# Optimization experiments

Measured on AMD Instinct MI355X. Metric: run time of the kernel, lower is better.

The kernel has to match this reference:

```python
import jax, jax.numpy as jnp
import numpy as np
import math

BS, T, C, H, W = 2, 3, 128, 48, 48
NH, NL, NPT, KS = 8, 3, 4, 3
DH = C // NH
LQ = T * H * W


def conv2d(x, w, b):
    y = jax.lax.conv_general_dilated(x, w, (1, 1), 'SAME', dimension_numbers=('NCHW', 'OIHW', 'NCHW'))
    return y + b[None, :, None, None]


def bilinear_sample(img, x, y, zeros_pad):
    # img: (B, C, H, W); x, y: (B, Q) pixel coords. zeros_pad -> grid_sample padding_mode='zeros', else 'border'.
    B, Cc, Hh, Ww = img.shape
    x0 = jnp.floor(x); y0 = jnp.floor(y)
    wx = x - x0; wy = y - y0
    flat = img.reshape(B, Cc, Hh * Ww)
    def corner(xi, yi, wgt):
        if zeros_pad:
            wgt = wgt * ((xi >= 0) & (xi <= Ww - 1) & (yi >= 0) & (yi <= Hh - 1)).astype(img.dtype)
        xc = jnp.clip(xi, 0, Ww - 1).astype(jnp.int32)
        yc = jnp.clip(yi, 0, Hh - 1).astype(jnp.int32)
        g = jnp.take_along_axis(flat, (yc * Ww + xc)[:, None, :], axis=2)  # (B, C, Q)
        return g * wgt[:, None, :]
    return (corner(x0, y0, (1 - wx) * (1 - wy)) + corner(x0 + 1, y0, wx * (1 - wy))
            + corner(x0, y0 + 1, (1 - wx) * wy) + corner(x0 + 1, y0 + 1, wx * wy))


def warp_w_mask(x, flo):
    # grid_sample(border, align_corners=True): normalized coords round-trip to raw pixel coords grid+flow
    B, Cc, Hh, Ww = x.shape
    vx = (jnp.arange(Ww, dtype=x.dtype)[None, None, :] + flo[:, 0]).reshape(B, -1)
    vy = (jnp.arange(Hh, dtype=x.dtype)[None, :, None] + flo[:, 1]).reshape(B, -1)
    out = bilinear_sample(x, vx, vy, False).reshape(B, Cc, Hh, Ww)
    m = bilinear_sample(jnp.ones((B, 1, Hh, Ww), x.dtype), vx, vy, True).reshape(B, 1, Hh, Ww)
    m = jnp.where(m < 0.999, 0.0, 1.0).astype(x.dtype)
    return out * m


def flow_guid_offset(ff, fb, off):
    N = off.shape[0]
    off = off.reshape(N, NL, H * W, NH, NL, NPT, 2)
    ff01, ff12 = ff[:, 0], ff[:, 1]
    ff02 = ff01 + warp_w_mask(ff12, ff01)
    fb10, fb21 = fb[:, 0], fb[:, 1]
    fb20 = fb21 + warp_w_mask(fb10, fb21)
    seq = lambda f: f.transpose(0, 2, 3, 1).reshape(N, H * W, 2)
    z = jnp.zeros((N, H * W, 2), off.dtype)
    adds = jnp.stack([
        jnp.stack([z, seq(ff01), seq(ff02)], axis=2),
        jnp.stack([seq(fb10), z, seq(ff12)], axis=2),
        jnp.stack([seq(fb20), seq(fb21), z], axis=2)], axis=1)  # (N, 3, HW, 3, 2)
    off = off + adds[:, :, :, None, :, None, :]
    return off.reshape(N, LQ, NH, NL, NPT, 2)


def reference(query, input_flatten, reference_points, flow_forward, flow_backward,
              w_off, b_off, w_attn, b_attn, w_val, b_val, w_out, b_out,
              input_spatial_shapes, input_level_start_index, input_padding_mask):
    bs, t, c, h, w = query.shape
    N = bs
    value = conv2d(input_flatten.reshape(bs * t, c, h, w), w_val, b_val)
    off = conv2d(query.reshape(bs * t, c, h, w), w_off, b_off)
    attn = conv2d(query.reshape(bs * t, c, h, w), w_attn, b_attn)
    tohw = lambda x: x.reshape(bs, t, -1, h * w).transpose(0, 1, 3, 2).reshape(bs, t * h * w, -1)
    value, off, attn = tohw(value), tohw(off), tohw(attn)
    value = jnp.where(input_padding_mask[..., None], 0.0, value)
    value = value.reshape(N, t * h * w, NH, DH)
    off = off.reshape(N, LQ, NH, NL, NPT, 2)
    off = flow_guid_offset(flow_forward, flow_backward, off)
    attn = jax.nn.softmax(attn.reshape(N, LQ, NH, NL * NPT), axis=-1).reshape(N, LQ, NH, NL, NPT)
    normalizer = jnp.stack([input_spatial_shapes[:, 1], input_spatial_shapes[:, 0]], -1).astype(query.dtype)
    loc = reference_points[:, :, None, :, None, :] + off / normalizer[None, None, None, :, None, :]
    # multi-level deformable sampling: grid_sample(bilinear, zeros padding, align_corners=False)
    vb = value.reshape(N, NL, h * w, NH, DH).transpose(0, 1, 3, 4, 2).reshape(N * NL * NH, DH, h, w)
    px = (loc[..., 0] * w - 0.5).transpose(0, 3, 2, 1, 4).reshape(N * NL * NH, LQ * NPT)
    py = (loc[..., 1] * h - 0.5).transpose(0, 3, 2, 1, 4).reshape(N * NL * NH, LQ * NPT)
    samp = bilinear_sample(vb, px, py, True).reshape(N, NL, NH, DH, LQ, NPT)
    out = jnp.einsum('nlhdqp,nqhlp->nqhd', samp, attn).reshape(N, LQ, c)
    out = out.reshape(bs, t, h, w, c).transpose(0, 1, 4, 2, 3).reshape(bs * t, c, h, w)
    out = conv2d(out, w_out, b_out).reshape(bs, t, c, h, w)
    return out


def setup_inputs():
    key = jax.random.key(0)
    ks = jax.random.split(key, 9)
    query = jax.random.normal(ks[0], (BS, T, C, H, W), jnp.float32)
    input_flatten = jax.random.normal(ks[1], (BS, T, C, H, W), jnp.float32)
    reference_points = jax.random.uniform(ks[2], (BS, LQ, NL, 2), jnp.float32)
    flow_forward = jax.random.normal(ks[3], (BS, 2, 2, H, W), jnp.float32) * 2.0
    flow_backward = jax.random.normal(ks[4], (BS, 2, 2, H, W), jnp.float32) * 2.0
    co = NH * NL * NPT * 2
    w_off = jax.random.normal(ks[5], (co, C, KS, KS), jnp.float32) * 0.01
    thetas = np.arange(NH, dtype=np.float32) * (2.0 * math.pi / NH)
    g = np.stack([np.cos(thetas), np.sin(thetas)], -1)
    g = g / np.abs(g).max(-1, keepdims=True)
    g = np.tile(g.reshape(NH, 1, 1, 2), (1, NL, NPT, 1)) * (np.arange(NPT, dtype=np.float32) + 1.0).reshape(1, 1, NPT, 1)
    b_off = jnp.asarray(g.reshape(-1))
    ca = NH * NL * NPT
    w_attn = jax.random.normal(ks[6], (ca, C, KS, KS), jnp.float32) * 0.01
    b_attn = jnp.zeros((ca,), jnp.float32)
    s = 1.0 / np.sqrt(C * KS * KS)
    w_val = jax.random.normal(ks[7], (C, C, KS, KS), jnp.float32) * s
    b_val = jnp.zeros((C,), jnp.float32)
    w_out = jax.random.normal(ks[8], (C, C, KS, KS), jnp.float32) * s
    b_out = jnp.zeros((C,), jnp.float32)
    input_spatial_shapes = jnp.array([[H, W]] * NL, jnp.int32)
    input_level_start_index = jnp.array([0, H * W, 2 * H * W], jnp.int32)
    input_padding_mask = jnp.zeros((BS, LQ), bool)
    return {'query': query, 'input_flatten': input_flatten, 'reference_points': reference_points,
            'flow_forward': flow_forward, 'flow_backward': flow_backward,
            'w_off': w_off, 'b_off': b_off, 'w_attn': w_attn, 'b_attn': b_attn,
            'w_val': w_val, 'b_val': b_val, 'w_out': w_out, 'b_out': b_out,
            'input_spatial_shapes': input_spatial_shapes,
            'input_level_start_index': input_level_start_index,
            'input_padding_mask': input_padding_mask}
```

## Files before the change

kernel.cpp:

```cpp
#include <hip/hip_runtime.h>
#include <math.h>

#define WID 48
#define HW 2304
#define PAD 50

typedef _Float16 half8 __attribute__((ext_vector_type(8)));
typedef _Float16 half2 __attribute__((ext_vector_type(2)));
typedef float f32x4 __attribute__((ext_vector_type(4)));

__device__ __forceinline__ void gload_lds16(const void* g, void* l) {
  __builtin_amdgcn_global_load_lds((const __attribute__((address_space(1))) void*)g,
                                   (__attribute__((address_space(3))) void*)l, 16, 0, 0);
}

__global__ __launch_bounds__(256) void prep_kernel(
    const float* __restrict__ q, const float* __restrict__ f,
    _Float16* __restrict__ xq, _Float16* __restrict__ xf,
    const float* __restrict__ wv, const float* __restrict__ wo,
    const float* __restrict__ wa, const float* __restrict__ wu,
    _Float16* __restrict__ wt,
    const float* __restrict__ ff, const float* __restrict__ fb,
    float* __restrict__ adds,
    _Float16* __restrict__ wsh) {
  __shared__ _Float16 plds[48 * 136];
  const int b = blockIdx.x;
  const int tid = threadIdx.x;

  if (b < 576) {
    const int buf = b / 288;
    const int rem = b - buf * 288;
    const int img = rem / 48, y = rem - img * 48;
    const float* src = buf ? f : q;
    _Float16* dst = buf ? xf : xq;

    const int c = tid >> 1;
    const int seg = tid & 1;
    const float* rowp = src + ((size_t)img * 128 + c) * HW + y * WID + seg * 24;
    f32x4 v[6];
#pragma unroll
    for (int k = 0; k < 6; ++k) v[k] = *(const f32x4*)(rowp + 4 * k);
#pragma unroll
    for (int k = 0; k < 6; ++k)
#pragma unroll
      for (int e = 0; e < 4; ++e)
        plds[(seg * 24 + 4 * k + e) * 136 + c] = (_Float16)v[k][e];
    __syncthreads();

    _Float16* dstp = dst + (((size_t)img * PAD + y + 1) * PAD + 1) * 128;
#pragma unroll
    for (int k = 0; k < 3; ++k) {
      int m = tid + 256 * k;
      int px = m >> 4, c0 = (m & 15) << 3;
      half8 h = *(const half8*)(plds + px * 136 + c0);
      *(half8*)(dstp + (size_t)m * 8) = h;
    }

  } else if (b < 3024) {
    int gi = (b - 576) * 256 + tid;
    if (gi >= 544 * 1152) return;
    int row = gi / 1152, k = gi - row * 1152;
    int tap = k >> 7, ci = k & 127;
    const float* src; int co;
    if (row < 128)      { src = wv; co = row; }
    else if (row < 320) { src = wo; co = row - 128; }
    else if (row < 416) { src = wa; co = row - 320; }
    else                { src = wu; co = row - 416; }
    wt[gi] = (_Float16)src[((size_t)co * 128 + ci) * 9 + tap];

  } else if (b < 3325) {
    int gi = (b - 3024) * 256 + tid;
    const int IMG_ELE = PAD * PAD * 128;
    half8 z = {};
    if (gi < 75264) {
      int bi = gi / 3136;
      int r = gi - bi * 3136;
      int p = r >> 4;
      int cc = (r & 15) << 3;
      int y, x;
      if (p < 50)       { y = 0;           x = p; }
      else if (p < 100) { y = 49;          x = p - 50; }
      else if (p < 148) { y = p - 100 + 1; x = 0; }
      else              { y = p - 148 + 1; x = 49; }
      *(half8*)(wsh + (size_t)bi * IMG_ELE + ((size_t)y * PAD + x) * 128 + cc) = z;
    } else if (gi < 76864) {
      int r = gi - 75264;
      *(half8*)(wsh + (size_t)24 * IMG_ELE + (size_t)r * 8) = z;
    }

  } else {
    int idx = (b - 3325) * 256 + tid;
    if (idx >= 2 * HW) return;
    int n = idx / HW, hw = idx - n * HW;
    int y = hw / WID, x = hw - y * WID;

    const float* F = ff + (size_t)n * 4 * HW;
    const float* B = fb + (size_t)n * 4 * HW;

    float ff01x = F[hw],          ff01y = F[HW + hw];
    float ff12x = F[2 * HW + hw], ff12y = F[3 * HW + hw];
    float fb10x = B[hw],          fb10y = B[HW + hw];
    float fb21x = B[2 * HW + hw], fb21y = B[3 * HW + hw];

    auto warp2 = [&](const float* cx, const float* cy, float flox, float floy,
                     float& ox, float& oy) {
      float sx = (float)x + flox, sy = (float)y + floy;
      float fx = floorf(sx), fy = floorf(sy);
      int x0 = (int)fx, y0 = (int)fy;
      float wx = sx - fx, wy = sy - fy;
      float w00 = (1.f - wx) * (1.f - wy), w10 = wx * (1.f - wy);
      float w01 = (1.f - wx) * wy,         w11 = wx * wy;
      auto inside = [](int xi, int yi) {
        return (xi >= 0 && xi <= WID - 1 && yi >= 0 && yi <= WID - 1) ? 1.f : 0.f;
      };
      float m = w00 * inside(x0, y0)     + w10 * inside(x0 + 1, y0) +
                w01 * inside(x0, y0 + 1) + w11 * inside(x0 + 1, y0 + 1);
      float mm = (m < 0.999f) ? 0.f : 1.f;
      auto cl = [](int v) { return v < 0 ? 0 : (v > WID - 1 ? WID - 1 : v); };
      int xa = cl(x0), xb = cl(x0 + 1), ya = cl(y0), yb = cl(y0 + 1);
      int i00 = ya * WID + xa, i10 = ya * WID + xb;
      int i01 = yb * WID + xa, i11 = yb * WID + xb;
      ox = mm * (w00 * cx[i00] + w10 * cx[i10] + w01 * cx[i01] + w11 * cx[i11]);
      oy = mm * (w00 * cy[i00] + w10 * cy[i10] + w01 * cy[i01] + w11 * cy[i11]);
    };

    float wfx, wfy;
    warp2(F + 2 * HW, F + 3 * HW, ff01x, ff01y, wfx, wfy);
    float ff02x = ff01x + wfx, ff02y = ff01y + wfy;
    float wbx, wby;
    warp2(B, B + HW, fb21x, fb21y, wbx, wby);
    float fb20x = fb21x + wbx, fb20y = fb21y + wby;

    auto W_ = [&](int t, int l, float vx, float vy) {
      size_t o = (((size_t)(n * 3 + t) * 3 + l) * HW + hw) * 2;
      adds[o] = vx; adds[o + 1] = vy;
    };
    W_(0, 0, 0.f, 0.f);     W_(0, 1, ff01x, ff01y); W_(0, 2, ff02x, ff02y);
    W_(1, 0, fb10x, fb10y); W_(1, 1, 0.f, 0.f);     W_(1, 2, ff12x, ff12y);
    W_(2, 0, fb20x, fb20y); W_(2, 1, fb21x, fb21y); W_(2, 2, 0.f, 0.f);
  }
}

#define CONV_BUF_ELE (96 * 64 + 64 * 64)

__device__ __forceinline__ void conv_body(
    int bx, const _Float16* __restrict__ xpad, const _Float16* __restrict__ wt,
    const float* __restrict__ bias0, const float* __restrict__ bias1, int bsplit,
    int CO, int co0, int layout, void* __restrict__ outp, _Float16* lds) {
  const int tid = threadIdx.x;
  const int w = tid >> 6, lane = tid & 63;
  const int img = bx / 24, rp = bx - img * 24;
  const int y0 = rp * 2;

  const int pxh = w & 1, coh = w >> 1;

  f32x4 acc[3][2] = {};

  const int lr8 = lane >> 3;
  const int lc  = lane & 7;

  auto stage = [&](int s, _Float16* l) {
    const int tap = s >> 1, ci0 = (s & 1) << 6;
    const int dy = tap / 3, dx = tap - dy * 3;
    _Float16* lA = l;
    _Float16* lB = l + 96 * 64;
#pragma unroll
    for (int it = 0; it < 3; ++it) {
      int i = w * 3 + it;
      int r = 8 * i + lr8;
      int cs = lc ^ (r & 7);
      int up = (r >= 48) ? 1 : 0;
      int yy = y0 + up + dy;
      int xx = (r - 48 * up) + dx;
      const _Float16* src = xpad + (((size_t)(img * PAD + yy)) * PAD + xx) * 128 + ci0 + cs * 8;
      gload_lds16(src, lA + i * 512);
    }
#pragma unroll
    for (int jt = 0; jt < 2; ++jt) {
      int j = w * 2 + jt;
      int r = 8 * j + lr8;
      int cs = lc ^ (r & 7);
      int co = co0 + r; if (co >= CO) co = CO - 1;
      const _Float16* src = wt + (size_t)co * 1152 + tap * 128 + ci0 + cs * 8;
      gload_lds16(src, lB + j * 512);
    }
  };

  stage(0, lds);
  stage(1, lds + CONV_BUF_ELE);
  asm volatile("s_waitcnt vmcnt(5)" ::: "memory");
  __builtin_amdgcn_s_barrier();

  const int lrow = lane & 15, lk = lane >> 4;
#pragma unroll
  for (int s = 0; s < 18; ++s) {
    _Float16* lA = lds + (s & 1) * CONV_BUF_ELE;
    _Float16* lB = lA + 96 * 64;

    __builtin_amdgcn_s_setprio(1);
#pragma unroll
    for (int sub = 0; sub < 2; ++sub) {
      int kc = sub * 4 + lk;
      half8 a[3], bb[2];
#pragma unroll
      for (int m = 0; m < 3; ++m) {
        int r = 48 * pxh + 16 * m + lrow;
        a[m] = *(const half8*)(lA + r * 64 + ((kc ^ (r & 7)) * 8));
      }
#pragma unroll
      for (int n = 0; n < 2; ++n) {
        int r = 32 * coh + 16 * n + lrow;
        bb[n] = *(const half8*)(lB + r * 64 + ((kc ^ (r & 7)) * 8));
      }
#pragma unroll
      for (int m = 0; m < 3; ++m)
#pragma unroll
        for (int n = 0; n < 2; ++n)
          acc[m][n] = __builtin_amdgcn_mfma_f32_16x16x32_f16(a[m], bb[n], acc[m][n], 0, 0, 0);
    }
    __builtin_amdgcn_s_setprio(0);

    if (s < 17) {
      __builtin_amdgcn_s_barrier();
      if (s + 2 < 18) {
        stage(s + 2, lA);
        asm volatile("s_waitcnt vmcnt(5)" ::: "memory");
      } else {
        asm volatile("s_waitcnt vmcnt(0)" ::: "memory");
      }
      __builtin_amdgcn_s_barrier();
    }
  }

  const int lg = lane >> 4;
#pragma unroll
  for (int m = 0; m < 3; ++m) {
#pragma unroll
    for (int n = 0; n < 2; ++n) {
      int co = co0 + 32 * coh + 16 * n + lrow;
      if (co >= CO) continue;
      float bv = (co < bsplit) ? bias0[co] : bias1[co - bsplit];
#pragma unroll
      for (int r = 0; r < 4; ++r) {
        int pl = 48 * pxh + 16 * m + 4 * lg + r;
        int pix = rp * 96 + pl;
        float v = acc[m][n][r] + bv;
        if (layout == 1) {
          ((_Float16*)outp)[((size_t)img * HW + pix) * CO + co] = (_Float16)v;
        } else if (layout == 2) {
          int yy = pix / WID, xx = pix - yy * WID;
          ((_Float16*)outp)[(((size_t)img * PAD + yy + 1) * PAD + xx + 1) * 128 + co] = (_Float16)v;
        } else {
          ((float*)outp)[((size_t)img * CO + co) * HW + pix] = v;
        }
      }
    }
  }
}

__global__ __launch_bounds__(256) void conv_offattn_value(
    const _Float16* __restrict__ xq, const _Float16* __restrict__ xf,
    const _Float16* __restrict__ wt,
    const float* __restrict__ b_off, const float* __restrict__ b_attn,
    const float* __restrict__ b_val,
    _Float16* __restrict__ offattn, _Float16* __restrict__ vpad) {
  __shared__ _Float16 lds[2 * CONV_BUF_ELE];
  const int y = blockIdx.y;
  if (y < 5) {
    conv_body(blockIdx.x, xq, wt + (size_t)128 * 1152, b_off, b_attn, 192,
              288, y * 64, 1, offattn, lds);
  } else {
    conv_body(blockIdx.x, xf, wt, b_val, b_val, 128,
              128, (y - 5) * 64, 2, vpad, lds);
  }
}

__global__ __launch_bounds__(256) void conv_out(
    const _Float16* __restrict__ xout, const _Float16* __restrict__ wt,
    const float* __restrict__ b_out, float* __restrict__ out) {
  __shared__ _Float16 lds[2 * CONV_BUF_ELE];
  conv_body(blockIdx.x, xout, wt, b_out, b_out, 128, 128, blockIdx.y * 64, 0,
            out, lds);
}

__global__ __launch_bounds__(256) void sample_kernel(
    const _Float16* __restrict__ vpad,
    const _Float16* __restrict__ offattn,
    const float* __restrict__ refpts, const float* __restrict__ adds,
    _Float16* __restrict__ xout) {
  __shared__ float Wlds[16][13][4];
  __shared__ int   IBlds[16][12];
  const int tid = threadIdx.x;
  const int pixg = blockIdx.x * 2 + (tid >> 7);
  const int g = tid >> 4;
  const int h = g & 7;
  const int d = tid & 15;
  const int img = pixg / HW, hw = pixg - img * HW;
  const int n = img / 3, t = img - n * 3;

  const _Float16* rec = offattn + ((size_t)img * HW + hw) * 288;

  const int i = (d < 12) ? d : 11;
  const int l = i >> 2;

  half2 o2 = *(const half2*)(rec + (h * 12 + i) * 2);
  float lgt = (float)rec[192 + h * 12 + i];
  if (d >= 12) lgt = -1e30f;

  const float* addp = adds + (((size_t)(n * 3 + t) * 3 + l) * HW + hw) * 2;
  const float* rp = refpts + ((size_t)(n * 3 + t) * HW + hw) * 6 + l * 2;

  float px = fmaf(rp[0], 48.f, -0.5f) + (float)o2[0] + addp[0];
  float py = fmaf(rp[1], 48.f, -0.5f) + (float)o2[1] + addp[1];
  px = fminf(fmaxf(px, -1.f), 48.f);
  py = fminf(fmaxf(py, -1.f), 48.f);
  float fx = floorf(px), fy = floorf(py);
  int x0 = (int)fx, y0 = (int)fy;
  float wx = px - fx, wy = py - fy;
  float w00 = (1.f - wx) * (1.f - wy), w10 = wx * (1.f - wy);
  float w01 = (1.f - wx) * wy,         w11 = wx * wy;

  float mx = lgt;
#pragma unroll
  for (int m = 8; m >= 1; m >>= 1) mx = fmaxf(mx, __shfl_xor(mx, m, 16));
  float e = __expf(lgt - mx);
  float s = e;
#pragma unroll
  for (int m = 8; m >= 1; m >>= 1) s += __shfl_xor(s, m, 16);
  float aw = e * __builtin_amdgcn_rcpf(s);
  w00 *= aw; w10 *= aw; w01 *= aw; w11 *= aw;

  int ib = (((n * 3 + l) * PAD + (y0 + 1)) * PAD + (x0 + 1)) * 128 + h * 16;

  if (d < 12) {
    f32x4 w4 = {w00, w10, w01, w11};
    *(f32x4*)&Wlds[g][d][0] = w4;
    IBlds[g][d] = ib;
  }
  __syncthreads();

  float acc = 0.f;
#pragma unroll
  for (int j = 0; j < 12; ++j) {
    f32x4 W = *(const f32x4*)&Wlds[g][j][0];
    int jb = IBlds[g][j];
    const _Float16* vp = vpad + jb + d;
    acc = fmaf(W[0], (float)vp[0], acc);
    acc = fmaf(W[1], (float)vp[128], acc);
    acc = fmaf(W[2], (float)vp[PAD * 128], acc);
    acc = fmaf(W[3], (float)vp[PAD * 128 + 128], acc);
  }

  int y = hw / WID, x = hw - y * WID;
  xout[(((size_t)img * PAD + y + 1) * PAD + x + 1) * 128 + h * 16 + d] = (_Float16)acc;
}

extern "C" void kernel_launch(void* const* d_in, const int* in_sizes, int n_in,
                              void* d_out, int out_size, void* d_ws, size_t ws_size,
                              hipStream_t stream) {
  const float* query         = (const float*)d_in[0];
  const float* input_flatten = (const float*)d_in[1];
  const float* refpts        = (const float*)d_in[2];
  const float* ff            = (const float*)d_in[3];
  const float* fb            = (const float*)d_in[4];
  const float* w_off         = (const float*)d_in[5];
  const float* b_off         = (const float*)d_in[6];
  const float* w_attn        = (const float*)d_in[7];
  const float* b_attn        = (const float*)d_in[8];
  const float* w_val         = (const float*)d_in[9];
  const float* b_val         = (const float*)d_in[10];
  const float* w_out         = (const float*)d_in[11];
  const float* b_out         = (const float*)d_in[12];
  float* out = (float*)d_out;

  char* ws = (char*)d_ws;
  const size_t PADSZ = (size_t)6 * PAD * PAD * 128 * sizeof(_Float16);
  const size_t GUARD = (size_t)2 * PAD * 128 * sizeof(_Float16);
  _Float16* xq      = (_Float16*)(ws);
  _Float16* xf      = (_Float16*)(ws + PADSZ);
  _Float16* xout    = (_Float16*)(ws + 2 * PADSZ);
  _Float16* vpad    = (_Float16*)(ws + 3 * PADSZ);
  _Float16* wt      = (_Float16*)(ws + 4 * PADSZ + GUARD);
  _Float16* offattn = (_Float16*)(ws + 4 * PADSZ + GUARD + 1253376);
  float*    adds    = (float*)   (ws + 4 * PADSZ + GUARD + 1253376 + 7962624);

  prep_kernel<<<3343, 256, 0, stream>>>(query, input_flatten, xq, xf,
                                        w_val, w_off, w_attn, w_out, wt,
                                        ff, fb, adds, (_Float16*)ws);

  conv_offattn_value<<<dim3(144, 7), 256, 0, stream>>>(xq, xf, wt,
                                                       b_off, b_attn, b_val,
                                                       offattn, vpad);

  sample_kernel<<<6912, 256, 0, stream>>>(vpad, offattn, refpts, adds, xout);

  conv_out<<<dim3(144, 2), 256, 0, stream>>>(xout, wt + (size_t)416 * 1152,
                                             b_out, out);
}
```

Before: 65.11 us.

## Pre-pack conv weights in MFMA fragment order and load B directly to registers

```diff
diff --git a/kernel.cpp b/kernel.cpp
--- a/kernel.cpp
+++ b/kernel.cpp
@@ -19,7 +19,7 @@
     _Float16* __restrict__ xq, _Float16* __restrict__ xf,
     const float* __restrict__ wv, const float* __restrict__ wo,
     const float* __restrict__ wa, const float* __restrict__ wu,
-    _Float16* __restrict__ wt,
+    _Float16* __restrict__ wtf,
     const float* __restrict__ ff, const float* __restrict__ fb,
     float* __restrict__ adds,
     _Float16* __restrict__ wsh) {
@@ -56,20 +56,32 @@
       *(half8*)(dstp + (size_t)m * 8) = h;
     }
 
-  } else if (b < 3024) {
-    int gi = (b - 576) * 256 + tid;
-    if (gi >= 544 * 1152) return;
-    int row = gi / 1152, k = gi - row * 1152;
-    int tap = k >> 7, ci = k & 127;
+  } else if (b < 3168) {
+    int gb = b - 576;
+    int g = gb / 288;
+    int off = (gb - g * 288) * 256 + tid;
+    int s    = off >> 12;
+    int coh  = (off >> 11) & 1;
+    int sub  = (off >> 10) & 1;
+    int nn   = (off >> 9) & 1;
+    int lane = (off >> 3) & 63;
+    int j    = off & 7;
+    int r  = 32 * coh + 16 * nn + (lane & 15);
+    int ci = ((s & 1) << 6) + (sub * 4 + (lane >> 4)) * 8 + j;
+    int tap = s >> 1;
     const float* src; int co;
-    if (row < 128)      { src = wv; co = row; }
-    else if (row < 320) { src = wo; co = row - 128; }
-    else if (row < 416) { src = wa; co = row - 320; }
-    else                { src = wu; co = row - 416; }
-    wt[gi] = (_Float16)src[((size_t)co * 128 + ci) * 9 + tap];
-
-  } else if (b < 3325) {
-    int gi = (b - 3024) * 256 + tid;
+    if (g < 5) {
+      co = g * 64 + r; if (co > 287) co = 287;
+      if (co < 192) { src = wo; } else { src = wa; co -= 192; }
+    } else if (g < 7) {
+      src = wv; co = (g - 5) * 64 + r;
+    } else {
+      src = wu; co = (g - 7) * 64 + r;
+    }
+    wtf[(size_t)g * 73728 + off] = (_Float16)src[((size_t)co * 128 + ci) * 9 + tap];
+
+  } else if (b < 3469) {
+    int gi = (b - 3168) * 256 + tid;
     const int IMG_ELE = PAD * PAD * 128;
     half8 z = {};
     if (gi < 75264) {
@@ -89,7 +101,7 @@
     }
 
   } else {
-    int idx = (b - 3325) * 256 + tid;
+    int idx = (b - 3469) * 256 + tid;
     if (idx >= 2 * HW) return;
     int n = idx / HW, hw = idx - n * HW;
     int y = hw / WID, x = hw - y * WID;
@@ -141,10 +153,10 @@
   }
 }
 
-#define CONV_BUF_ELE (96 * 64 + 64 * 64)
+#define CONV_ABUF 6144
 
 __device__ __forceinline__ void conv_body(
-    int bx, const _Float16* __restrict__ xpad, const _Float16* __restrict__ wt,
+    int bx, const _Float16* __restrict__ xpad, const _Float16* __restrict__ wtfg,
     const float* __restrict__ bias0, const float* __restrict__ bias1, int bsplit,
     int CO, int co0, int layout, void* __restrict__ outp, _Float16* lds) {
   const int tid = threadIdx.x;
@@ -159,11 +171,9 @@
   const int lr8 = lane >> 3;
   const int lc  = lane & 7;
 
-  auto stage = [&](int s, _Float16* l) {
+  auto stageA = [&](int s, _Float16* l) {
     const int tap = s >> 1, ci0 = (s & 1) << 6;
     const int dy = tap / 3, dx = tap - dy * 3;
-    _Float16* lA = l;
-    _Float16* lB = l + 96 * 64;
 #pragma unroll
     for (int it = 0; it < 3; ++it) {
       int i = w * 3 + it;
@@ -173,60 +183,62 @@
       int yy = y0 + up + dy;
       int xx = (r - 48 * up) + dx;
       const _Float16* src = xpad + (((size_t)(img * PAD + yy)) * PAD + xx) * 128 + ci0 + cs * 8;
-      gload_lds16(src, lA + i * 512);
-    }
-#pragma unroll
-    for (int jt = 0; jt < 2; ++jt) {
-      int j = w * 2 + jt;
-      int r = 8 * j + lr8;
-      int cs = lc ^ (r & 7);
-      int co = co0 + r; if (co >= CO) co = CO - 1;
-      const _Float16* src = wt + (size_t)co * 1152 + tap * 128 + ci0 + cs * 8;
-      gload_lds16(src, lB + j * 512);
+      gload_lds16(src, l + i * 512);
     }
   };
 
-  stage(0, lds);
-  stage(1, lds + CONV_BUF_ELE);
-  asm volatile("s_waitcnt vmcnt(5)" ::: "memory");
+  const _Float16* wb = wtfg + coh * 2048 + lane * 8;
+
+  half8 bf[2][2][2];
+#pragma unroll
+  for (int sub = 0; sub < 2; ++sub)
+#pragma unroll
+    for (int nn = 0; nn < 2; ++nn)
+      bf[0][sub][nn] = *(const half8*)(wb + sub * 1024 + nn * 512);
+  stageA(0, lds);
+  stageA(1, lds + CONV_ABUF);
+  asm volatile("s_waitcnt vmcnt(3)" ::: "memory");
   __builtin_amdgcn_s_barrier();
 
   const int lrow = lane & 15, lk = lane >> 4;
 #pragma unroll
   for (int s = 0; s < 18; ++s) {
-    _Float16* lA = lds + (s & 1) * CONV_BUF_ELE;
-    _Float16* lB = lA + 96 * 64;
-
+    if (s < 17) {
+#pragma unroll
+      for (int sub = 0; sub < 2; ++sub)
+#pragma unroll
+        for (int nn = 0; nn < 2; ++nn)
+          bf[(s + 1) & 1][sub][nn] =
+              *(const half8*)(wb + (s + 1) * 4096 + sub * 1024 + nn * 512);
+    }
+
+    _Float16* lA = lds + (s & 1) * CONV_ABUF;
     __builtin_amdgcn_s_setprio(1);
 #pragma unroll
     for (int sub = 0; sub < 2; ++sub) {
       int kc = sub * 4 + lk;
-      half8 a[3], bb[2];
+      half8 a[3];
 #pragma unroll
       for (int m = 0; m < 3; ++m) {
         int r = 48 * pxh + 16 * m + lrow;
         a[m] = *(const half8*)(lA + r * 64 + ((kc ^ (r & 7)) * 8));
       }
 #pragma unroll
-      for (int n = 0; n < 2; ++n) {
-        int r = 32 * coh + 16 * n + lrow;
-        bb[n] = *(const half8*)(lB + r * 64 + ((kc ^ (r & 7)) * 8));
-      }
-#pragma unroll
       for (int m = 0; m < 3; ++m)
 #pragma unroll
         for (int n = 0; n < 2; ++n)
-          acc[m][n] = __builtin_amdgcn_mfma_f32_16x16x32_f16(a[m], bb[n], acc[m][n], 0, 0, 0);
+          acc[m][n] = __builtin_amdgcn_mfma_f32_16x16x32_f16(
+              a[m], bf[s & 1][sub][n], acc[m][n], 0, 0, 0);
     }
     __builtin_amdgcn_s_setprio(0);
 
     if (s < 17) {
       __builtin_amdgcn_s_barrier();
       if (s + 2 < 18) {
-        stage(s + 2, lA);
-        asm volatile("s_waitcnt vmcnt(5)" ::: "memory");
+        stageA(s + 2, lA);
+        asm volatile("s_waitcnt vmcnt(7)" ::: "memory");
       } else {
-        asm volatile("s_waitcnt vmcnt(0)" ::: "memory");
+        asm volatile("s_waitcnt vmcnt(4)" ::: "memory");
       }
       __builtin_amdgcn_s_barrier();
     }
@@ -260,27 +272,27 @@
 
 __global__ __launch_bounds__(256) void conv_offattn_value(
     const _Float16* __restrict__ xq, const _Float16* __restrict__ xf,
-    const _Float16* __restrict__ wt,
+    const _Float16* __restrict__ wtf,
     const float* __restrict__ b_off, const float* __restrict__ b_attn,
     const float* __restrict__ b_val,
     _Float16* __restrict__ offattn, _Float16* __restrict__ vpad) {
-  __shared__ _Float16 lds[2 * CONV_BUF_ELE];
+  __shared__ _Float16 lds[2 * CONV_ABUF];
   const int y = blockIdx.y;
   if (y < 5) {
-    conv_body(blockIdx.x, xq, wt + (size_t)128 * 1152, b_off, b_attn, 192,
+    conv_body(blockIdx.x, xq, wtf + (size_t)y * 73728, b_off, b_attn, 192,
               288, y * 64, 1, offattn, lds);
   } else {
-    conv_body(blockIdx.x, xf, wt, b_val, b_val, 128,
+    conv_body(blockIdx.x, xf, wtf + (size_t)y * 73728, b_val, b_val, 128,
               128, (y - 5) * 64, 2, vpad, lds);
   }
 }
 
 __global__ __launch_bounds__(256) void conv_out(
-    const _Float16* __restrict__ xout, const _Float16* __restrict__ wt,
+    const _Float16* __restrict__ xout, const _Float16* __restrict__ wtf,
     const float* __restrict__ b_out, float* __restrict__ out) {
-  __shared__ _Float16 lds[2 * CONV_BUF_ELE];
-  conv_body(blockIdx.x, xout, wt, b_out, b_out, 128, 128, blockIdx.y * 64, 0,
-            out, lds);
+  __shared__ _Float16 lds[2 * CONV_ABUF];
+  conv_body(blockIdx.x, xout, wtf + (size_t)(7 + blockIdx.y) * 73728,
+            b_out, b_out, 128, 128, blockIdx.y * 64, 0, out, lds);
 }
 
 __global__ __launch_bounds__(256) void sample_kernel(
@@ -376,24 +388,24 @@
   char* ws = (char*)d_ws;
   const size_t PADSZ = (size_t)6 * PAD * PAD * 128 * sizeof(_Float16);
   const size_t GUARD = (size_t)2 * PAD * 128 * sizeof(_Float16);
+  const size_t WTFSZ = (size_t)9 * 73728 * sizeof(_Float16);
   _Float16* xq      = (_Float16*)(ws);
   _Float16* xf      = (_Float16*)(ws + PADSZ);
   _Float16* xout    = (_Float16*)(ws + 2 * PADSZ);
   _Float16* vpad    = (_Float16*)(ws + 3 * PADSZ);
-  _Float16* wt      = (_Float16*)(ws + 4 * PADSZ + GUARD);
-  _Float16* offattn = (_Float16*)(ws + 4 * PADSZ + GUARD + 1253376);
-  float*    adds    = (float*)   (ws + 4 * PADSZ + GUARD + 1253376 + 7962624);
-
-  prep_kernel<<<3343, 256, 0, stream>>>(query, input_flatten, xq, xf,
-                                        w_val, w_off, w_attn, w_out, wt,
+  _Float16* wtf     = (_Float16*)(ws + 4 * PADSZ + GUARD);
+  _Float16* offattn = (_Float16*)(ws + 4 * PADSZ + GUARD + WTFSZ);
+  float*    adds    = (float*)   (ws + 4 * PADSZ + GUARD + WTFSZ + 7962624);
+
+  prep_kernel<<<3487, 256, 0, stream>>>(query, input_flatten, xq, xf,
+                                        w_val, w_off, w_attn, w_out, wtf,
                                         ff, fb, adds, (_Float16*)ws);
 
-  conv_offattn_value<<<dim3(144, 7), 256, 0, stream>>>(xq, xf, wt,
+  conv_offattn_value<<<dim3(144, 7), 256, 0, stream>>>(xq, xf, wtf,
                                                        b_off, b_attn, b_val,
                                                        offattn, vpad);
 
   sample_kernel<<<6912, 256, 0, stream>>>(vpad, offattn, refpts, adds, xout);
 
-  conv_out<<<dim3(144, 2), 256, 0, stream>>>(xout, wt + (size_t)416 * 1152,
-                                             b_out, out);
-}
+  conv_out<<<dim3(144, 2), 256, 0, stream>>>(xout, wtf, b_out, out);
+}
```

Result: slower. 70.58 us (+8.4%).
